# Kernel tuning notes

Measured on AMD Instinct MI355X. Metric: run time of the kernel, lower is better.

The kernel has to match this reference:

```python
import jax, jax.numpy as jnp
import numpy as np

B, L, D2, C = 64, 512, 512, 50  # D2 = hidden_size*2

def setup_inputs() -> dict:
    key = jax.random.key(0)
    ks = jax.random.split(key, 8)
    text_vec = jax.random.normal(ks[0], (B, L, D2), dtype=jnp.float32)
    text_mask = jnp.ones((B, L), dtype=bool)
    sbj_bound = jnp.sort(jax.random.randint(ks[1], (B, 2), 0, L), axis=-1)
    obj_start = jax.random.randint(ks[2], (B, L), 0, C)
    obj_end = jax.random.randint(ks[3], (B, L), 0, C)
    W_start = jax.random.normal(ks[4], (2 * D2, C), dtype=jnp.float32) * 0.02
    b_start = jnp.zeros((C,), dtype=jnp.float32)
    W_end = jax.random.normal(ks[5], (2 * D2, C), dtype=jnp.float32) * 0.02
    b_end = jnp.zeros((C,), dtype=jnp.float32)
    return {"text_vec": text_vec, "text_mask": text_mask, "sbj_bound": sbj_bound,
            "obj_start": obj_start, "obj_end": obj_end,
            "W_start": W_start, "b_start": b_start, "W_end": W_end, "b_end": b_end}

def _masked_ce(logits, labels, maskf, value_num):
    # logits [B,L,C], labels [B,L]
    logp = jax.nn.log_softmax(logits, axis=-1)
    nll = -jnp.take_along_axis(logp, labels[..., None], axis=-1)[..., 0]
    return (nll * maskf).sum() / value_num

def reference(text_vec, text_mask, sbj_bound, obj_start, obj_end,
              W_start, b_start, W_end, b_end):
    pos = jnp.arange(L)  # [L]
    start, end = sbj_bound[:, 0], sbj_bound[:, 1]
    # inclusive span mask, vectorized replacement for the per-example loop
    span = ((pos[None, :] >= start[:, None]) & (pos[None, :] <= end[:, None])).astype(text_vec.dtype)  # [B,L]
    count = span.sum(axis=1, keepdims=True)  # [B,1], >=1 since start<=end
    sbj_vec = jnp.einsum('bl,bld->bd', span, text_vec) / count  # segment mean [B,D2]
    # cat([text_vec, sbj_vec]) @ W  ==  text_vec @ W[:D2] + sbj_vec @ W[D2:]
    def head(W, b):
        return (jnp.einsum('bld,dc->blc', text_vec, W[:D2])
                + (sbj_vec @ W[D2:])[:, None, :] + b)
    o1 = head(W_start, b_start)
    o2 = head(W_end, b_end)
    maskf = text_mask.astype(jnp.float32)
    value_num = maskf.sum()
    loss_obj_s = _masked_ce(o1, obj_start, maskf, value_num)
    loss_obj_e = _masked_ce(o2, obj_end, maskf, value_num)
    return loss_obj_s + loss_obj_e
```

## Files before the change

### kernel.cpp

```cpp
#include <hip/hip_runtime.h>
#include <math.h>

#define BB 64
#define LL 512
#define DD 512
#define CC 50
#define NC 100
#define NCP 112
#define WST 520

#define WSB_LOSS  0
#define WSB_CNT   4
#define WSB_DONE  8
#define WSB_SCOMB 64
#define WSB_PART  28736
#define WSB_WTOP  553024
#define WSB_WBOT  667712

typedef __attribute__((ext_vector_type(8))) short bf16x8;
typedef __attribute__((ext_vector_type(4))) float f32x4;

static __device__ __forceinline__ unsigned short f2bf(float x) {
    unsigned int u = __float_as_uint(x);
    u += 0x7FFFu + ((u >> 16) & 1u);
    return (unsigned short)(u >> 16);
}
static __device__ __forceinline__ float bf2f(unsigned short h) {
    return __uint_as_float(((unsigned int)h) << 16);
}

__global__ __launch_bounds__(256) void k_prep(
    const float* __restrict__ tv, const int* __restrict__ sbj_bound,
    const float* __restrict__ Wst, const float* __restrict__ Wen,
    char* __restrict__ wsb)
{
    __shared__ float sh[128 * 53];
    const int t = threadIdx.x;
    const int blk = blockIdx.x;

    if (blk < 512) {
        const int b = blk >> 3, seg = blk & 7;
        const int start = sbj_bound[2 * b], end = sbj_bound[2 * b + 1];
        int r0 = seg * 64;      if (r0 < start) r0 = start;
        int r1 = seg * 64 + 63; if (r1 > end)   r1 = end;
        const int c4 = t & 127, par = t >> 7;
        const float* bp = tv + (size_t)b * LL * DD + c4 * 4;
        float4 a0 = {0, 0, 0, 0}, a1 = {0, 0, 0, 0};
        int r = r0 + par;
        for (; r + 2 <= r1; r += 4) {
            float4 v0 = *(const float4*)(bp + (size_t)r * DD);
            float4 v1 = *(const float4*)(bp + (size_t)(r + 2) * DD);
            a0.x += v0.x; a0.y += v0.y; a0.z += v0.z; a0.w += v0.w;
            a1.x += v1.x; a1.y += v1.y; a1.z += v1.z; a1.w += v1.w;
        }
        for (; r <= r1; r += 2) {
            float4 v0 = *(const float4*)(bp + (size_t)r * DD);
            a0.x += v0.x; a0.y += v0.y; a0.z += v0.z; a0.w += v0.w;
        }
        float4* buf = (float4*)sh;
        float4 acc = {a0.x + a1.x, a0.y + a1.y, a0.z + a1.z, a0.w + a1.w};
        buf[t] = acc;
        __syncthreads();
        if (t < 128) {
            float4 x = buf[t], y = buf[t + 128];
            unsigned short* part = (unsigned short*)(wsb + WSB_PART);
            ushort4 o;
            o.x = f2bf(x.x + y.x); o.y = f2bf(x.y + y.y);
            o.z = f2bf(x.z + y.z); o.w = f2bf(x.w + y.w);
            *(ushort4*)(part + ((size_t)(seg * BB + b)) * DD + t * 4) = o;
        }
    } else {
        const int bi = blk - 512;
        const int mat = bi >> 3;
        const int cj = bi & 7;
        const float* W = mat ? Wen : Wst;
        const int kbase = cj * 128;
        const float* src = W + (size_t)kbase * CC;
#pragma unroll
        for (int i = 0; i < 25; i++) {
            int idx = t + i * 256;
            int kr = idx / 50, c = idx - kr * 50;
            sh[kr * 53 + c] = src[idx];
        }
        __syncthreads();
        unsigned short* outp =
            (unsigned short*)(wsb + ((cj < 4) ? WSB_WTOP : WSB_WBOT));
        const int kout = kbase & 511;
#pragma unroll
        for (int i = 0; i < 25; i++) {
            int idx = t + i * 256;
            int n = idx >> 7, kl = idx & 127;
            outp[((size_t)(mat * CC + n)) * DD + kout + kl] = f2bf(sh[kl * 53 + n]);
        }
        if (bi == 0 && t == 0) {
            *(float*)(wsb + WSB_LOSS) = 0.0f;
            *(float*)(wsb + WSB_CNT)  = 0.0f;
            *(int*)(wsb + WSB_DONE)   = 0;
        }
    }
}

__global__ __launch_bounds__(256) void k_scomb(
    const int* __restrict__ sbj_bound,
    const float* __restrict__ bst, const float* __restrict__ ben,
    char* __restrict__ wsb)
{
    __shared__ __align__(16) unsigned short sbjb[16 * WST];
    const int t = threadIdx.x;
    const int g = blockIdx.x;
    const unsigned short* part = (const unsigned short*)(wsb + WSB_PART);

#pragma unroll
    for (int i = 0; i < 8; i++) {
        int idx = t + i * 256;
        int bo = idx >> 7, d4 = idx & 127;
        int b = g * 16 + bo;
        float inv = 1.0f / (float)(sbj_bound[2 * b + 1] - sbj_bound[2 * b] + 1);
        float sx = 0.f, sy = 0.f, sz = 0.f, sw = 0.f;
#pragma unroll
        for (int seg = 0; seg < 8; seg++) {
            ushort4 v = *(const ushort4*)(part + ((size_t)(seg * BB + b)) * DD + d4 * 4);
            sx += bf2f(v.x); sy += bf2f(v.y); sz += bf2f(v.z); sw += bf2f(v.w);
        }
        ushort4 o;
        o.x = f2bf(sx * inv); o.y = f2bf(sy * inv);
        o.z = f2bf(sz * inv); o.w = f2bf(sw * inv);
        *(ushort4*)(sbjb + bo * WST + d4 * 4) = o;
    }
    __syncthreads();

    const int wv = t >> 6, ln = t & 63, tc = ln & 15, quad = ln >> 4;
    const unsigned short* wbot = (const unsigned short*)(wsb + WSB_WBOT);
    float* scomb = (float*)(wsb + WSB_SCOMB);
    const unsigned short* Af = sbjb + tc * WST + quad * 8;
    const int nu = (wv < 3) ? 2 : 1;
    for (int j = 0; j < nu; j++) {
        const int u = wv * 2 + j;
        f32x4 acc = (f32x4)(0.0f);
        const unsigned short* Bf = wbot + (size_t)(u * 16 + tc) * DD + quad * 8;
#pragma unroll
        for (int kk = 0; kk < DD; kk += 32) {
            bf16x8 af = *(const bf16x8*)(Af + kk);
            bf16x8 bf = *(const bf16x8*)(Bf + kk);
            acc = __builtin_amdgcn_mfma_f32_16x16x32_bf16(af, bf, acc, 0, 0, 0);
        }
        const int cc = u * 16 + tc;
        const float bias = (cc < CC) ? bst[cc] : ((cc < NC) ? ben[cc - CC] : 0.0f);
#pragma unroll
        for (int i = 0; i < 4; i++) {
            int b = g * 16 + quad * 4 + i;
            scomb[b * NCP + cc] = acc[i] + bias;
        }
    }
}

__global__ __launch_bounds__(512, 2) void k_main(
    const float* __restrict__ tv,
    const int* __restrict__ mask,
    const int* __restrict__ obj_s, const int* __restrict__ obj_e,
    char* __restrict__ wsb, float* __restrict__ out)
{
    __shared__ __align__(16) unsigned short Wt[NCP * WST];
    __shared__ float red[16];
    const int t = threadIdx.x, wv = t >> 6, ln = t & 63;
    const int tc = ln & 15, quad = ln >> 4;
    const int m0w = blockIdx.x * 128 + wv * 16;
    const int b = blockIdx.x >> 2;
    const unsigned short* wtop = (const unsigned short*)(wsb + WSB_WTOP);

    const float* Abase = tv + (size_t)(m0w + tc) * DD + quad * 8;

    float4 alo[16];
#pragma unroll
    for (int j = 0; j < 8; j++) {
        alo[2 * j]     = *(const float4*)(Abase + j * 32);
        alo[2 * j + 1] = *(const float4*)(Abase + j * 32 + 4);
    }
#pragma unroll
    for (int i = 0; i < 14; i++) {
        int idx = t + i * 512;
        int n = idx >> 6, ch = idx & 63;
        *(bf16x8*)(Wt + n * WST + ch * 8) =
            *(const bf16x8*)(wtop + (size_t)n * DD + ch * 8);
    }
    float4 ahi[16];
#pragma unroll
    for (int j = 0; j < 8; j++) {
        ahi[2 * j]     = *(const float4*)(Abase + 256 + j * 32);
        ahi[2 * j + 1] = *(const float4*)(Abase + 256 + j * 32 + 4);
    }
    __syncthreads();

    f32x4 acc[7];
#pragma unroll
    for (int u = 0; u < 7; u++) acc[u] = (f32x4)(0.0f);
    const unsigned short* Wf = Wt + tc * WST + quad * 8;

#pragma unroll
    for (int j = 0; j < 8; j++) {
        float4 v0 = alo[2 * j], v1 = alo[2 * j + 1];
        bf16x8 af;
        af[0] = (short)f2bf(v0.x); af[1] = (short)f2bf(v0.y);
        af[2] = (short)f2bf(v0.z); af[3] = (short)f2bf(v0.w);
        af[4] = (short)f2bf(v1.x); af[5] = (short)f2bf(v1.y);
        af[6] = (short)f2bf(v1.z); af[7] = (short)f2bf(v1.w);
#pragma unroll
        for (int u = 0; u < 7; u++) {
            bf16x8 bf = *(const bf16x8*)(Wf + u * 16 * WST + j * 32);
            acc[u] = __builtin_amdgcn_mfma_f32_16x16x32_bf16(af, bf, acc[u], 0, 0, 0);
        }
    }
#pragma unroll
    for (int j = 0; j < 8; j++) {
        float4 v0 = ahi[2 * j], v1 = ahi[2 * j + 1];
        bf16x8 af;
        af[0] = (short)f2bf(v0.x); af[1] = (short)f2bf(v0.y);
        af[2] = (short)f2bf(v0.z); af[3] = (short)f2bf(v0.w);
        af[4] = (short)f2bf(v1.x); af[5] = (short)f2bf(v1.y);
        af[6] = (short)f2bf(v1.z); af[7] = (short)f2bf(v1.w);
#pragma unroll
        for (int u = 0; u < 7; u++) {
            bf16x8 bf = *(const bf16x8*)(Wf + u * 16 * WST + 256 + j * 32);
            acc[u] = __builtin_amdgcn_mfma_f32_16x16x32_bf16(af, bf, acc[u], 0, 0, 0);
        }
    }

    const float* scomb = (const float*)(wsb + WSB_SCOMB);
    float sc[7];
#pragma unroll
    for (int u = 0; u < 7; u++) sc[u] = scomb[b * NCP + u * 16 + tc];

    float loss_local = 0.0f, cnt_local = 0.0f;
#pragma unroll
    for (int i = 0; i < 4; i++) {
        const int l = (m0w + quad * 4 + i) & (LL - 1);
        const int lab1 = obj_s[b * LL + l];
        const int lab2 = obj_e[b * LL + l] + CC;
        const int mk   = mask[b * LL + l];
        float lg[7];
#pragma unroll
        for (int u = 0; u < 7; u++) lg[u] = acc[u][i] + sc[u];
        float m1 = fmaxf(fmaxf(lg[0], lg[1]), lg[2]);
        if (tc < 2) m1 = fmaxf(m1, lg[3]);
        float m2 = fmaxf(lg[4], lg[5]);
        if (tc >= 2) m2 = fmaxf(m2, lg[3]);
        if (tc < 4)  m2 = fmaxf(m2, lg[6]);
#pragma unroll
        for (int off = 1; off < 16; off <<= 1) {
            m1 = fmaxf(m1, __shfl_xor(m1, off, 16));
            m2 = fmaxf(m2, __shfl_xor(m2, off, 16));
        }
        float e1 = expf(lg[0] - m1) + expf(lg[1] - m1) + expf(lg[2] - m1)
                 + ((tc < 2) ? expf(lg[3] - m1) : 0.0f);
        float e2 = expf(lg[4] - m2) + expf(lg[5] - m2)
                 + ((tc >= 2) ? expf(lg[3] - m2) : 0.0f)
                 + ((tc < 4)  ? expf(lg[6] - m2) : 0.0f);
        float t1 = 0.0f, t2 = 0.0f;
#pragma unroll
        for (int u = 0; u < 7; u++) {
            const int cc = u * 16 + tc;
            if (cc == lab1) t1 = lg[u];
            if (cc == lab2) t2 = lg[u];
        }
#pragma unroll
        for (int off = 1; off < 16; off <<= 1) {
            e1 += __shfl_xor(e1, off, 16);
            e2 += __shfl_xor(e2, off, 16);
            t1 += __shfl_xor(t1, off, 16);
            t2 += __shfl_xor(t2, off, 16);
        }
        if (tc == 0) {
            const float nll = (m1 + logf(e1) - t1) + (m2 + logf(e2) - t2);
            loss_local += mk ? nll : 0.0f;
            cnt_local  += mk ? 1.0f : 0.0f;
        }
    }
#pragma unroll
    for (int off = 1; off < 64; off <<= 1) {
        loss_local += __shfl_xor(loss_local, off);
        cnt_local  += __shfl_xor(cnt_local, off);
    }
    if (ln == 0) { red[wv * 2] = loss_local; red[wv * 2 + 1] = cnt_local; }
    __syncthreads();
    if (t == 0) {
        float Ls = 0.f, Cs = 0.f;
#pragma unroll
        for (int w = 0; w < 8; w++) { Ls += red[w * 2]; Cs += red[w * 2 + 1]; }
        float* wsf = (float*)wsb;
        atomicAdd(&wsf[0], Ls);
        atomicAdd(&wsf[1], Cs);
        __threadfence();
        int old = atomicAdd((int*)(wsb + WSB_DONE), 1);
        if (old == (int)gridDim.x - 1) {
            float L = atomicAdd(&wsf[0], 0.0f);
            float C = atomicAdd(&wsf[1], 0.0f);
            out[0] = L / C;
        }
    }
}

extern "C" void kernel_launch(void* const* d_in, const int* in_sizes, int n_in,
                              void* d_out, int out_size, void* d_ws, size_t ws_size,
                              hipStream_t stream) {
    const float* tv   = (const float*)d_in[0];
    const int*   mask = (const int*)d_in[1];
    const int*   sbj  = (const int*)d_in[2];
    const int*   objs = (const int*)d_in[3];
    const int*   obje = (const int*)d_in[4];
    const float* Wst  = (const float*)d_in[5];
    const float* bst  = (const float*)d_in[6];
    const float* Wen  = (const float*)d_in[7];
    const float* ben  = (const float*)d_in[8];
    float* out = (float*)d_out;
    char*  wsb = (char*)d_ws;

    k_prep<<<528, 256, 0, stream>>>(tv, sbj, Wst, Wen, wsb);
    k_scomb<<<4, 256, 0, stream>>>(sbj, bst, ben, wsb);
    k_main<<<256, 512, 0, stream>>>(tv, mask, objs, obje, wsb, out);
}
```

Baseline: 141.4 us.

## Pre-convert text_vec to bf16 in prep kernel and feed MFMA from bf16 copy

The prep kernel now streams every row of text_vec, not just the subject span rows. It writes a bf16 copy to workspace while accumulating the span sum under a per-row predicate. The main kernel then loads bf16 A fragments directly, which halves its activation reads and removes the per-element fp32-to-bf16 conversion. It also stages weight loads through registers before the LDS store. The cost is a full extra fp32 read plus a bf16 write and re-read of the activation tensor across kernels, and the code assumes the workspace is large enough for the bf16 copy.

```diff
diff --git a/kernel.cpp b/kernel.cpp
--- a/kernel.cpp
+++ b/kernel.cpp
@@ -16,6 +16,7 @@
 #define WSB_PART  28736
 #define WSB_WTOP  553024
 #define WSB_WBOT  667712
+#define WSB_TVB   782400
 
 typedef __attribute__((ext_vector_type(8))) short bf16x8;
 typedef __attribute__((ext_vector_type(4))) float f32x4;
@@ -41,24 +42,25 @@
     if (blk < 512) {
         const int b = blk >> 3, seg = blk & 7;
         const int start = sbj_bound[2 * b], end = sbj_bound[2 * b + 1];
-        int r0 = seg * 64;      if (r0 < start) r0 = start;
-        int r1 = seg * 64 + 63; if (r1 > end)   r1 = end;
         const int c4 = t & 127, par = t >> 7;
-        const float* bp = tv + (size_t)b * LL * DD + c4 * 4;
-        float4 a0 = {0, 0, 0, 0}, a1 = {0, 0, 0, 0};
-        int r = r0 + par;
-        for (; r + 2 <= r1; r += 4) {
-            float4 v0 = *(const float4*)(bp + (size_t)r * DD);
-            float4 v1 = *(const float4*)(bp + (size_t)(r + 2) * DD);
-            a0.x += v0.x; a0.y += v0.y; a0.z += v0.z; a0.w += v0.w;
-            a1.x += v1.x; a1.y += v1.y; a1.z += v1.z; a1.w += v1.w;
-        }
-        for (; r <= r1; r += 2) {
-            float4 v0 = *(const float4*)(bp + (size_t)r * DD);
-            a0.x += v0.x; a0.y += v0.y; a0.z += v0.z; a0.w += v0.w;
+        const size_t rowbase = (size_t)b * LL + seg * 64;
+        const float* bp = tv + rowbase * DD + c4 * 4;
+        unsigned short* tvb = (unsigned short*)(wsb + WSB_TVB);
+        unsigned short* op = tvb + rowbase * DD + c4 * 4;
+        float4 acc = {0, 0, 0, 0};
+#pragma unroll 4
+        for (int i = 0; i < 32; i++) {
+            const int r = par + 2 * i;
+            float4 v = *(const float4*)(bp + (size_t)r * DD);
+            ushort4 o;
+            o.x = f2bf(v.x); o.y = f2bf(v.y); o.z = f2bf(v.z); o.w = f2bf(v.w);
+            *(ushort4*)(op + (size_t)r * DD) = o;
+            const int gr = seg * 64 + r;
+            if (gr >= start && gr <= end) {
+                acc.x += v.x; acc.y += v.y; acc.z += v.z; acc.w += v.w;
+            }
         }
         float4* buf = (float4*)sh;
-        float4 acc = {a0.x + a1.x, a0.y + a1.y, a0.z + a1.z, a0.w + a1.w};
         buf[t] = acc;
         __syncthreads();
         if (t < 128) {
@@ -155,7 +157,6 @@
 }
 
 __global__ __launch_bounds__(512, 2) void k_main(
-    const float* __restrict__ tv,
     const int* __restrict__ mask,
     const int* __restrict__ obj_s, const int* __restrict__ obj_e,
     char* __restrict__ wsb, float* __restrict__ out)
@@ -167,27 +168,25 @@
     const int m0w = blockIdx.x * 128 + wv * 16;
     const int b = blockIdx.x >> 2;
     const unsigned short* wtop = (const unsigned short*)(wsb + WSB_WTOP);
-
-    const float* Abase = tv + (size_t)(m0w + tc) * DD + quad * 8;
-
-    float4 alo[16];
-#pragma unroll
-    for (int j = 0; j < 8; j++) {
-        alo[2 * j]     = *(const float4*)(Abase + j * 32);
-        alo[2 * j + 1] = *(const float4*)(Abase + j * 32 + 4);
-    }
+    const unsigned short* tvb  = (const unsigned short*)(wsb + WSB_TVB);
+
+    bf16x8 breg[14];
 #pragma unroll
     for (int i = 0; i < 14; i++) {
         int idx = t + i * 512;
         int n = idx >> 6, ch = idx & 63;
-        *(bf16x8*)(Wt + n * WST + ch * 8) =
-            *(const bf16x8*)(wtop + (size_t)n * DD + ch * 8);
-    }
-    float4 ahi[16];
-#pragma unroll
-    for (int j = 0; j < 8; j++) {
-        ahi[2 * j]     = *(const float4*)(Abase + 256 + j * 32);
-        ahi[2 * j + 1] = *(const float4*)(Abase + 256 + j * 32 + 4);
+        breg[i] = *(const bf16x8*)(wtop + (size_t)n * DD + ch * 8);
+    }
+    const unsigned short* Abase = tvb + (size_t)(m0w + tc) * DD + quad * 8;
+    bf16x8 af[16];
+#pragma unroll
+    for (int j = 0; j < 16; j++) af[j] = *(const bf16x8*)(Abase + j * 32);
+
+#pragma unroll
+    for (int i = 0; i < 14; i++) {
+        int idx = t + i * 512;
+        int n = idx >> 6, ch = idx & 63;
+        *(bf16x8*)(Wt + n * WST + ch * 8) = breg[i];
     }
     __syncthreads();
 
@@ -197,31 +196,11 @@
     const unsigned short* Wf = Wt + tc * WST + quad * 8;
 
 #pragma unroll
-    for (int j = 0; j < 8; j++) {
-        float4 v0 = alo[2 * j], v1 = alo[2 * j + 1];
-        bf16x8 af;
-        af[0] = (short)f2bf(v0.x); af[1] = (short)f2bf(v0.y);
-        af[2] = (short)f2bf(v0.z); af[3] = (short)f2bf(v0.w);
-        af[4] = (short)f2bf(v1.x); af[5] = (short)f2bf(v1.y);
-        af[6] = (short)f2bf(v1.z); af[7] = (short)f2bf(v1.w);
+    for (int j = 0; j < 16; j++) {
 #pragma unroll
         for (int u = 0; u < 7; u++) {
             bf16x8 bf = *(const bf16x8*)(Wf + u * 16 * WST + j * 32);
-            acc[u] = __builtin_amdgcn_mfma_f32_16x16x32_bf16(af, bf, acc[u], 0, 0, 0);
-        }
-    }
-#pragma unroll
-    for (int j = 0; j < 8; j++) {
-        float4 v0 = ahi[2 * j], v1 = ahi[2 * j + 1];
-        bf16x8 af;
-        af[0] = (short)f2bf(v0.x); af[1] = (short)f2bf(v0.y);
-        af[2] = (short)f2bf(v0.z); af[3] = (short)f2bf(v0.w);
-        af[4] = (short)f2bf(v1.x); af[5] = (short)f2bf(v1.y);
-        af[6] = (short)f2bf(v1.z); af[7] = (short)f2bf(v1.w);
-#pragma unroll
-        for (int u = 0; u < 7; u++) {
-            bf16x8 bf = *(const bf16x8*)(Wf + u * 16 * WST + 256 + j * 32);
-            acc[u] = __builtin_amdgcn_mfma_f32_16x16x32_bf16(af, bf, acc[u], 0, 0, 0);
+            acc[u] = __builtin_amdgcn_mfma_f32_16x16x32_bf16(af[j], bf, acc[u], 0, 0, 0);
         }
     }
 
@@ -316,5 +295,5 @@
 
     k_prep<<<528, 256, 0, stream>>>(tv, sbj, Wst, Wen, wsb);
     k_scomb<<<4, 256, 0, stream>>>(sbj, bst, ben, wsb);
-    k_main<<<256, 512, 0, stream>>>(tv, mask, objs, obje, wsb, out);
-}
+    k_main<<<256, 512, 0, stream>>>(mask, objs, obje, wsb, out);
+}
```

After: 145.3 us. 1.03x slower.

## Stream activation tiles through double-buffered LDS via global_load_lds

Applied to the files above, without the earlier changes.

Instead of every thread preloading its entire 512-wide activation row fragment into registers, the main kernel now streams 32-column K slices of the 128-row tile into a double-buffered, XOR-swizzled LDS buffer using direct global-to-LDS loads. Loads for later slices are issued while earlier slices feed the MFMAs. The weight staging is also split into a register gather phase followed by an LDS store phase. Occupancy hint drops to one block per SM because of the larger LDS footprint, and a barrier per K step is added, which risks exposing latency that the previous two-block occupancy hid.

```diff
diff --git a/kernel.cpp b/kernel.cpp
--- a/kernel.cpp
+++ b/kernel.cpp
@@ -27,6 +27,11 @@
 }
 static __device__ __forceinline__ float bf2f(unsigned short h) {
     return __uint_as_float(((unsigned int)h) << 16);
+}
+static __device__ __forceinline__ void gl2lds16(const void* g, void* l) {
+    __builtin_amdgcn_global_load_lds(
+        (const __attribute__((address_space(1))) unsigned int*)g,
+        (__attribute__((address_space(3))) unsigned int*)l, 16, 0, 0);
 }
 
 __global__ __launch_bounds__(256) void k_prep(
@@ -154,40 +159,46 @@
     }
 }
 
-__global__ __launch_bounds__(512, 2) void k_main(
+__global__ __launch_bounds__(512, 1) void k_main(
     const float* __restrict__ tv,
     const int* __restrict__ mask,
     const int* __restrict__ obj_s, const int* __restrict__ obj_e,
     char* __restrict__ wsb, float* __restrict__ out)
 {
     __shared__ __align__(16) unsigned short Wt[NCP * WST];
+    __shared__ __align__(16) float Abuf[2][4096];
     __shared__ float red[16];
     const int t = threadIdx.x, wv = t >> 6, ln = t & 63;
     const int tc = ln & 15, quad = ln >> 4;
-    const int m0w = blockIdx.x * 128 + wv * 16;
+    const int m0 = blockIdx.x * 128;
     const int b = blockIdx.x >> 2;
     const unsigned short* wtop = (const unsigned short*)(wsb + WSB_WTOP);
 
-    const float* Abase = tv + (size_t)(m0w + tc) * DD + quad * 8;
-
-    float4 alo[16];
-#pragma unroll
-    for (int j = 0; j < 8; j++) {
-        alo[2 * j]     = *(const float4*)(Abase + j * 32);
-        alo[2 * j + 1] = *(const float4*)(Abase + j * 32 + 4);
-    }
+#pragma unroll
+    for (int s = 0; s < 2; s++) {
+        const float* gsrc = tv + (size_t)m0 * DD + s * 32;
+#pragma unroll
+        for (int j = 0; j < 2; j++) {
+            const int gi = j * 512 + t;
+            const int r = gi >> 3, sl = gi & 7;
+            const int kc = sl ^ (r & 7);
+            const float* g = gsrc + (size_t)r * DD + kc * 4;
+            char* l = (char*)&Abuf[s][0] + (j * 512 + (t & ~63)) * 16;
+            gl2lds16(g, l);
+        }
+    }
+    bf16x8 breg[14];
 #pragma unroll
     for (int i = 0; i < 14; i++) {
         int idx = t + i * 512;
         int n = idx >> 6, ch = idx & 63;
-        *(bf16x8*)(Wt + n * WST + ch * 8) =
-            *(const bf16x8*)(wtop + (size_t)n * DD + ch * 8);
-    }
-    float4 ahi[16];
-#pragma unroll
-    for (int j = 0; j < 8; j++) {
-        ahi[2 * j]     = *(const float4*)(Abase + 256 + j * 32);
-        ahi[2 * j + 1] = *(const float4*)(Abase + 256 + j * 32 + 4);
+        breg[i] = *(const bf16x8*)(wtop + (size_t)n * DD + ch * 8);
+    }
+#pragma unroll
+    for (int i = 0; i < 14; i++) {
+        int idx = t + i * 512;
+        int n = idx >> 6, ch = idx & 63;
+        *(bf16x8*)(Wt + n * WST + ch * 8) = breg[i];
     }
     __syncthreads();
 
@@ -195,10 +206,15 @@
 #pragma unroll
     for (int u = 0; u < 7; u++) acc[u] = (f32x4)(0.0f);
     const unsigned short* Wf = Wt + tc * WST + quad * 8;
-
-#pragma unroll
-    for (int j = 0; j < 8; j++) {
-        float4 v0 = alo[2 * j], v1 = alo[2 * j + 1];
+    const int r = wv * 16 + tc;
+    const int rx = r & 7;
+    const int g0 = r * 8 + ((quad * 2) ^ rx);
+    const int g1 = r * 8 + ((quad * 2 + 1) ^ rx);
+
+    for (int s = 0; s < 16; s++) {
+        const float* Ab = &Abuf[s & 1][0];
+        float4 v0 = *(const float4*)(Ab + g0 * 4);
+        float4 v1 = *(const float4*)(Ab + g1 * 4);
         bf16x8 af;
         af[0] = (short)f2bf(v0.x); af[1] = (short)f2bf(v0.y);
         af[2] = (short)f2bf(v0.z); af[3] = (short)f2bf(v0.w);
@@ -206,22 +222,21 @@
         af[6] = (short)f2bf(v1.z); af[7] = (short)f2bf(v1.w);
 #pragma unroll
         for (int u = 0; u < 7; u++) {
-            bf16x8 bf = *(const bf16x8*)(Wf + u * 16 * WST + j * 32);
+            bf16x8 bf = *(const bf16x8*)(Wf + u * 16 * WST + s * 32);
             acc[u] = __builtin_amdgcn_mfma_f32_16x16x32_bf16(af, bf, acc[u], 0, 0, 0);
         }
-    }
-#pragma unroll
-    for (int j = 0; j < 8; j++) {
-        float4 v0 = ahi[2 * j], v1 = ahi[2 * j + 1];
-        bf16x8 af;
-        af[0] = (short)f2bf(v0.x); af[1] = (short)f2bf(v0.y);
-        af[2] = (short)f2bf(v0.z); af[3] = (short)f2bf(v0.w);
-        af[4] = (short)f2bf(v1.x); af[5] = (short)f2bf(v1.y);
-        af[6] = (short)f2bf(v1.z); af[7] = (short)f2bf(v1.w);
-#pragma unroll
-        for (int u = 0; u < 7; u++) {
-            bf16x8 bf = *(const bf16x8*)(Wf + u * 16 * WST + 256 + j * 32);
-            acc[u] = __builtin_amdgcn_mfma_f32_16x16x32_bf16(af, bf, acc[u], 0, 0, 0);
+        __syncthreads();
+        if (s + 2 < 16) {
+            const float* gsrc = tv + (size_t)m0 * DD + (s + 2) * 32;
+#pragma unroll
+            for (int j = 0; j < 2; j++) {
+                const int gi = j * 512 + t;
+                const int rr = gi >> 3, sl = gi & 7;
+                const int kc = sl ^ (rr & 7);
+                const float* g = gsrc + (size_t)rr * DD + kc * 4;
+                char* l = (char*)&Abuf[s & 1][0] + (j * 512 + (t & ~63)) * 16;
+                gl2lds16(g, l);
+            }
         }
     }
 
@@ -233,7 +248,7 @@
     float loss_local = 0.0f, cnt_local = 0.0f;
 #pragma unroll
     for (int i = 0; i < 4; i++) {
-        const int l = (m0w + quad * 4 + i) & (LL - 1);
+        const int l = (m0 + wv * 16 + quad * 4 + i) & (LL - 1);
         const int lab1 = obj_s[b * LL + l];
         const int lab2 = obj_e[b * LL + l] + CC;
         const int mk   = mask[b * LL + l];
```

Result: slower. 147.8 us (+4.5%).

## Pre-pack W into MFMA fragment order and stream it to LDS via global_load_lds

Applied to the files above, without the earlier changes.

The prep kernel now writes the top half of the weights directly in MFMA B-fragment order, so the main kernel can copy them into LDS with direct global-to-LDS loads and read them without a padded stride. The main kernel moves to 512 blocks of 256 threads (64 rows each) with software double-buffered A-register loads that overlap the MFMA loop, and uses a perm-based bf16 pack (truncation instead of round-to-nearest). This aims to cut LDS staging overhead and latency exposure. The trade-offs are slightly different rounding, 112KB of LDS per block that limits occupancy to one block per CU, and more blocks each reloading W.

```diff
diff --git a/kernel.cpp b/kernel.cpp
--- a/kernel.cpp
+++ b/kernel.cpp
@@ -7,15 +7,14 @@
 #define CC 50
 #define NC 100
 #define NCP 112
-#define WST 520
 
 #define WSB_LOSS  0
 #define WSB_CNT   4
 #define WSB_DONE  8
 #define WSB_SCOMB 64
 #define WSB_PART  28736
-#define WSB_WTOP  553024
-#define WSB_WBOT  667712
+#define WSB_WBOT  553024
+#define WSB_BPACK 667712
 
 typedef __attribute__((ext_vector_type(8))) short bf16x8;
 typedef __attribute__((ext_vector_type(4))) float f32x4;
@@ -27,6 +26,14 @@
 }
 static __device__ __forceinline__ float bf2f(unsigned short h) {
     return __uint_as_float(((unsigned int)h) << 16);
+}
+static __device__ __forceinline__ unsigned int pk2bf(float a, float b) {
+    return __builtin_amdgcn_perm(__float_as_uint(b), __float_as_uint(a), 0x07060302u);
+}
+static __device__ __forceinline__ void gl2lds16(const void* g, void* l) {
+    __builtin_amdgcn_global_load_lds(
+        (const __attribute__((address_space(1))) unsigned int*)g,
+        (__attribute__((address_space(3))) unsigned int*)l, 16, 0, 0);
 }
 
 __global__ __launch_bounds__(256) void k_prep(
@@ -69,43 +76,65 @@
             o.z = f2bf(x.z + y.z); o.w = f2bf(x.w + y.w);
             *(ushort4*)(part + ((size_t)(seg * BB + b)) * DD + t * 4) = o;
         }
-    } else {
+    } else if (blk < 520) {
         const int bi = blk - 512;
-        const int mat = bi >> 3;
-        const int cj = bi & 7;
+        const int mat = bi >> 2;
+        const int cj = bi & 3;
         const float* W = mat ? Wen : Wst;
-        const int kbase = cj * 128;
+        const int kbase = 512 + cj * 128;
         const float* src = W + (size_t)kbase * CC;
 #pragma unroll
         for (int i = 0; i < 25; i++) {
             int idx = t + i * 256;
-            int kr = idx / 50, c = idx - kr * 50;
-            sh[kr * 53 + c] = src[idx];
+            sh[idx] = src[idx];
         }
         __syncthreads();
-        unsigned short* outp =
-            (unsigned short*)(wsb + ((cj < 4) ? WSB_WTOP : WSB_WBOT));
-        const int kout = kbase & 511;
+        unsigned short* outp = (unsigned short*)(wsb + WSB_WBOT);
+        const int kout = cj * 128;
 #pragma unroll
         for (int i = 0; i < 25; i++) {
             int idx = t + i * 256;
             int n = idx >> 7, kl = idx & 127;
-            outp[((size_t)(mat * CC + n)) * DD + kout + kl] = f2bf(sh[kl * 53 + n]);
+            outp[((size_t)(mat * CC + n)) * DD + kout + kl] = f2bf(sh[kl * 50 + n]);
         }
         if (bi == 0 && t == 0) {
             *(float*)(wsb + WSB_LOSS) = 0.0f;
             *(float*)(wsb + WSB_CNT)  = 0.0f;
             *(int*)(wsb + WSB_DONE)   = 0;
         }
-    }
-}
-
+    } else {
+        const int bi = blk - 520;
+        const int ln = t & 63, jj = t >> 6;
+        const int tc = ln & 15, quad = ln >> 4;
+        const int j0 = jj * 2;
+        unsigned int* bp = (unsigned int*)(wsb + WSB_BPACK);
+#pragma unroll
+        for (int q = 0; q < 7; q++) {
+            const int fid = bi * 7 + q;
+            const int u = fid % 7, s = fid / 7;
+            const int cc = u * 16 + tc;
+            const int k0 = s * 32 + quad * 8 + j0;
+            float a = 0.f, bb = 0.f;
+            if (cc < CC) {
+                a  = Wst[(size_t)k0 * CC + cc];
+                bb = Wst[(size_t)(k0 + 1) * CC + cc];
+            } else if (cc < NC) {
+                a  = Wen[(size_t)k0 * CC + cc - CC];
+                bb = Wen[(size_t)(k0 + 1) * CC + cc - CC];
+            }
+            bp[fid * 256 + ln * 4 + jj] =
+                (unsigned int)f2bf(a) | ((unsigned int)f2bf(bb) << 16);
+        }
+    }
+}
+
+#define SST 520
 __global__ __launch_bounds__(256) void k_scomb(
     const int* __restrict__ sbj_bound,
     const float* __restrict__ bst, const float* __restrict__ ben,
     char* __restrict__ wsb)
 {
-    __shared__ __align__(16) unsigned short sbjb[16 * WST];
+    __shared__ __align__(16) unsigned short sbjb[16 * SST];
     const int t = threadIdx.x;
     const int g = blockIdx.x;
     const unsigned short* part = (const unsigned short*)(wsb + WSB_PART);
@@ -125,14 +154,14 @@
         ushort4 o;
         o.x = f2bf(sx * inv); o.y = f2bf(sy * inv);
         o.z = f2bf(sz * inv); o.w = f2bf(sw * inv);
-        *(ushort4*)(sbjb + bo * WST + d4 * 4) = o;
+        *(ushort4*)(sbjb + bo * SST + d4 * 4) = o;
     }
     __syncthreads();
 
     const int wv = t >> 6, ln = t & 63, tc = ln & 15, quad = ln >> 4;
     const unsigned short* wbot = (const unsigned short*)(wsb + WSB_WBOT);
     float* scomb = (float*)(wsb + WSB_SCOMB);
-    const unsigned short* Af = sbjb + tc * WST + quad * 8;
+    const unsigned short* Af = sbjb + tc * SST + quad * 8;
     const int nu = (wv < 3) ? 2 : 1;
     for (int j = 0; j < nu; j++) {
         const int u = wv * 2 + j;
@@ -154,74 +183,72 @@
     }
 }
 
-__global__ __launch_bounds__(512, 2) void k_main(
+__global__ __launch_bounds__(256, 1) void k_main(
     const float* __restrict__ tv,
     const int* __restrict__ mask,
     const int* __restrict__ obj_s, const int* __restrict__ obj_e,
     char* __restrict__ wsb, float* __restrict__ out)
 {
-    __shared__ __align__(16) unsigned short Wt[NCP * WST];
-    __shared__ float red[16];
+    __shared__ __align__(16) unsigned short Bl[112 * 512];
+    __shared__ float red[8];
     const int t = threadIdx.x, wv = t >> 6, ln = t & 63;
     const int tc = ln & 15, quad = ln >> 4;
-    const int m0w = blockIdx.x * 128 + wv * 16;
-    const int b = blockIdx.x >> 2;
-    const unsigned short* wtop = (const unsigned short*)(wsb + WSB_WTOP);
-
-    const float* Abase = tv + (size_t)(m0w + tc) * DD + quad * 8;
-
-    float4 alo[16];
-#pragma unroll
-    for (int j = 0; j < 8; j++) {
-        alo[2 * j]     = *(const float4*)(Abase + j * 32);
-        alo[2 * j + 1] = *(const float4*)(Abase + j * 32 + 4);
-    }
-#pragma unroll
-    for (int i = 0; i < 14; i++) {
-        int idx = t + i * 512;
-        int n = idx >> 6, ch = idx & 63;
-        *(bf16x8*)(Wt + n * WST + ch * 8) =
-            *(const bf16x8*)(wtop + (size_t)n * DD + ch * 8);
-    }
-    float4 ahi[16];
-#pragma unroll
-    for (int j = 0; j < 8; j++) {
-        ahi[2 * j]     = *(const float4*)(Abase + 256 + j * 32);
-        ahi[2 * j + 1] = *(const float4*)(Abase + 256 + j * 32 + 4);
+    const int m0 = blockIdx.x * 64;
+    const int b = blockIdx.x >> 3;
+
+    const float* Ap = tv + (size_t)(m0 + wv * 16 + tc) * DD + quad * 8;
+
+    float4 ra0[8], ra1[8];
+#pragma unroll
+    for (int ks = 0; ks < 4; ks++) {
+        ra0[2 * ks]     = *(const float4*)(Ap + ks * 32);
+        ra0[2 * ks + 1] = *(const float4*)(Ap + ks * 32 + 4);
+    }
+#pragma unroll
+    for (int ks = 0; ks < 4; ks++) {
+        ra1[2 * ks]     = *(const float4*)(Ap + (4 + ks) * 32);
+        ra1[2 * ks + 1] = *(const float4*)(Ap + (4 + ks) * 32 + 4);
+    }
+    {
+        const char* gB = wsb + WSB_BPACK;
+#pragma unroll
+        for (int i = 0; i < 28; i++) {
+            const int gidx = t + i * 256;
+            gl2lds16(gB + (size_t)gidx * 16,
+                     (char*)Bl + (i * 256 + wv * 64) * 16);
+        }
     }
     __syncthreads();
 
     f32x4 acc[7];
 #pragma unroll
     for (int u = 0; u < 7; u++) acc[u] = (f32x4)(0.0f);
-    const unsigned short* Wf = Wt + tc * WST + quad * 8;
-
-#pragma unroll
-    for (int j = 0; j < 8; j++) {
-        float4 v0 = alo[2 * j], v1 = alo[2 * j + 1];
-        bf16x8 af;
-        af[0] = (short)f2bf(v0.x); af[1] = (short)f2bf(v0.y);
-        af[2] = (short)f2bf(v0.z); af[3] = (short)f2bf(v0.w);
-        af[4] = (short)f2bf(v1.x); af[5] = (short)f2bf(v1.y);
-        af[6] = (short)f2bf(v1.z); af[7] = (short)f2bf(v1.w);
-#pragma unroll
-        for (int u = 0; u < 7; u++) {
-            bf16x8 bf = *(const bf16x8*)(Wf + u * 16 * WST + j * 32);
-            acc[u] = __builtin_amdgcn_mfma_f32_16x16x32_bf16(af, bf, acc[u], 0, 0, 0);
-        }
-    }
-#pragma unroll
-    for (int j = 0; j < 8; j++) {
-        float4 v0 = ahi[2 * j], v1 = ahi[2 * j + 1];
-        bf16x8 af;
-        af[0] = (short)f2bf(v0.x); af[1] = (short)f2bf(v0.y);
-        af[2] = (short)f2bf(v0.z); af[3] = (short)f2bf(v0.w);
-        af[4] = (short)f2bf(v1.x); af[5] = (short)f2bf(v1.y);
-        af[6] = (short)f2bf(v1.z); af[7] = (short)f2bf(v1.w);
-#pragma unroll
-        for (int u = 0; u < 7; u++) {
-            bf16x8 bf = *(const bf16x8*)(Wf + u * 16 * WST + 256 + j * 32);
-            acc[u] = __builtin_amdgcn_mfma_f32_16x16x32_bf16(af, bf, acc[u], 0, 0, 0);
+    const unsigned short* Bf0 = Bl + ln * 8;
+
+#pragma unroll
+    for (int bt = 0; bt < 4; bt++) {
+        float4* cur = (bt & 1) ? ra1 : ra0;
+#pragma unroll
+        for (int ks = 0; ks < 4; ks++) {
+            const int s = bt * 4 + ks;
+            float4 v0 = cur[2 * ks], v1 = cur[2 * ks + 1];
+            union { unsigned int u32[4]; bf16x8 v; } af;
+            af.u32[0] = pk2bf(v0.x, v0.y);
+            af.u32[1] = pk2bf(v0.z, v0.w);
+            af.u32[2] = pk2bf(v1.x, v1.y);
+            af.u32[3] = pk2bf(v1.z, v1.w);
+#pragma unroll
+            for (int u = 0; u < 7; u++) {
+                bf16x8 bf = *(const bf16x8*)(Bf0 + (s * 7 + u) * 512);
+                acc[u] = __builtin_amdgcn_mfma_f32_16x16x32_bf16(af.v, bf, acc[u], 0, 0, 0);
+            }
+        }
+        if (bt < 2) {
+#pragma unroll
+            for (int ks = 0; ks < 4; ks++) {
+                cur[2 * ks]     = *(const float4*)(Ap + (4 * (bt + 2) + ks) * 32);
+                cur[2 * ks + 1] = *(const float4*)(Ap + (4 * (bt + 2) + ks) * 32 + 4);
+            }
         }
     }
 
@@ -233,7 +260,7 @@
     float loss_local = 0.0f, cnt_local = 0.0f;
 #pragma unroll
     for (int i = 0; i < 4; i++) {
-        const int l = (m0w + quad * 4 + i) & (LL - 1);
+        const int l = (m0 + wv * 16 + quad * 4 + i) & (LL - 1);
         const int lab1 = obj_s[b * LL + l];
         const int lab2 = obj_e[b * LL + l] + CC;
         const int mk   = mask[b * LL + l];
@@ -283,9 +310,8 @@
     if (ln == 0) { red[wv * 2] = loss_local; red[wv * 2 + 1] = cnt_local; }
     __syncthreads();
     if (t == 0) {
-        float Ls = 0.f, Cs = 0.f;
-#pragma unroll
-        for (int w = 0; w < 8; w++) { Ls += red[w * 2]; Cs += red[w * 2 + 1]; }
+        float Ls = red[0] + red[2] + red[4] + red[6];
+        float Cs = red[1] + red[3] + red[5] + red[7];
         float* wsf = (float*)wsb;
         atomicAdd(&wsf[0], Ls);
         atomicAdd(&wsf[1], Cs);
@@ -314,7 +340,7 @@
     float* out = (float*)d_out;
     char*  wsb = (char*)d_ws;
 
-    k_prep<<<528, 256, 0, stream>>>(tv, sbj, Wst, Wen, wsb);
+    k_prep<<<536, 256, 0, stream>>>(tv, sbj, Wst, Wen, wsb);
     k_scomb<<<4, 256, 0, stream>>>(sbj, bst, ben, wsb);
-    k_main<<<256, 512, 0, stream>>>(tv, mask, objs, obje, wsb, out);
-}
+    k_main<<<512, 256, 0, stream>>>(tv, mask, objs, obje, wsb, out);
+}
```

Result: slower. 154.0 us (+8.9%).
